# Kernel optimization log

Hardware: AMD Instinct MI355X
Metric: run time of the kernel (lower is better)

Reference implementation:

```python
import jax, jax.numpy as jnp
import numpy as np
import math

B, N, E, H, D = 8, 1024, 1024, 16, 64  # batch, node_cnt, embedding_dim, head_num, qkv_dim
SQRT_E, SQRT_D, CLIP = 32.0, 8.0, 10.0
MAX_PERIOD = 10000.0


def setup_inputs() -> dict:
    key = jax.random.key(0)
    ks = jax.random.split(key, 16)
    s = 0.03  # weight scale keeps tanh/softmax in a sane range
    return {
        "t": jax.random.uniform(ks[0], (B,), jnp.float32),
        "encoded_jobs": jax.random.normal(ks[1], (B, N, E), jnp.float32) * 0.5,
        "xt": jax.random.uniform(ks[2], (B, N, N), jnp.float32),
        "Wq": jax.random.normal(ks[3], (H * D, E), jnp.float32) * s,
        "Wk": jax.random.normal(ks[4], (H * D, E), jnp.float32) * s,
        "Wv": jax.random.normal(ks[5], (H * D, E), jnp.float32) * s,
        "Wc": jax.random.normal(ks[6], (E, H * D), jnp.float32) * s,
        "bc": jnp.zeros((E,), jnp.float32),
        "conv_w": jax.random.normal(ks[7], (2, 2), jnp.float32) * 0.5,  # 1x1 Conv2d(2,2)
        "conv_b": jnp.zeros((2,), jnp.float32),
        "tW1": jax.random.normal(ks[8], (E // 2, E), jnp.float32) * s,
        "tb1": jnp.zeros((E // 2,), jnp.float32),
        "tW2": jax.random.normal(ks[9], (E, E // 2), jnp.float32) * s,
        "tb2": jnp.zeros((E,), jnp.float32),
    }


def _timestep_embedding(t):
    half = E // 2
    freqs = jnp.exp(-math.log(MAX_PERIOD) * jnp.arange(half, dtype=jnp.float32) / half)
    args = t[:, None] * freqs[None, :]               # [B, E/2]
    return jnp.concatenate([jnp.cos(args), jnp.sin(args)], axis=-1)  # [B, E]


def reference(t, encoded_jobs, xt, Wq, Wk, Wv, Wc, bc, conv_w, conv_b, tW1, tb1, tW2, tb2):
    # time embedding MLP
    t_emb = jax.nn.relu(_timestep_embedding(t) @ tW1.T + tb1) @ tW2.T + tb2  # [B, E]

    def heads(W):
        return (encoded_jobs @ W.T).reshape(B, N, H, D).transpose(0, 2, 1, 3)  # [B,H,N,D]

    q, k, v = heads(Wq), heads(Wk), heads(Wv)
    attn = jax.nn.softmax(jnp.einsum('bhnd,bhmd->bhnm', q, k) / SQRT_D, axis=-1)
    out = jnp.einsum('bhnm,bhmd->bhnd', attn, v)
    out_concat = out.transpose(0, 2, 1, 3).reshape(B, N, H * D)
    mh = out_concat @ Wc.T + bc + t_emb[:, None, :]          # [B,N,E]

    # single-head score against encoded_jobs^T, scaled + tanh-clipped
    score = jnp.einsum('bne,bme->bnm', mh, encoded_jobs) / SQRT_E
    score_clipped = CLIP * jnp.tanh(score)

    stacked = jnp.stack([score_clipped, xt], axis=1)         # [B,2,N,N]
    conv_out = jnp.einsum('oi,binm->bonm', conv_w, stacked) + conv_b[None, :, None, None]
    return jax.nn.softmax(conv_out.transpose(0, 2, 3, 1), axis=3)  # [B,N,N,2]
```

## Files before the change

### kernel.cpp

```cpp
#include <hip/hip_runtime.h>
#include <hip/hip_bf16.h>
#include <math.h>

#define B_ 8
#define N_ 1024
#define E_ 1024
#define H_ 16
#define D_ 64

typedef __attribute__((ext_vector_type(8))) short short8;
typedef __attribute__((ext_vector_type(4))) float f32x4;

static __device__ __forceinline__ unsigned short f2bf(float f) {
    __hip_bfloat16 h = __float2bfloat16(f);
    return __builtin_bit_cast(unsigned short, h);
}
static __device__ __forceinline__ unsigned int cvtpk_bf16(float a, float b) {
    unsigned int r;
    asm("v_cvt_pk_bf16_f32 %0, %1, %2" : "=v"(r) : "v"(a), "v"(b));
    return r;
}
static __device__ __forceinline__ void gld_lds16(const void* g, void* l) {
    __builtin_amdgcn_global_load_lds(
        (const __attribute__((address_space(1))) unsigned int*)g,
        (__attribute__((address_space(3))) unsigned int*)l, 16, 0, 0);
}

__global__ __launch_bounds__(256) void cvt_fused(
    const float* __restrict__ ej, const float* __restrict__ w0,
    const float* __restrict__ w1, const float* __restrict__ w2,
    const float* __restrict__ w3,
    unsigned short* __restrict__ ejd, unsigned short* __restrict__ d0,
    unsigned short* __restrict__ d1, unsigned short* __restrict__ d2,
    unsigned short* __restrict__ d3,
    const float* __restrict__ t, const float* __restrict__ tW1,
    const float* __restrict__ tb1, float* __restrict__ h1T)
{
    const int gid = blockIdx.x;
    const int tid = threadIdx.x;
    if (gid < 12288) {
        const float* s; unsigned short* d; int i;
        if (gid < 8192) {
            s = ej; d = ejd; i = (gid * 256 + tid) * 4;
        } else {
            int w = (gid - 8192) >> 10;
            s = w == 0 ? w0 : (w == 1 ? w1 : (w == 2 ? w2 : w3));
            d = w == 0 ? d0 : (w == 1 ? d1 : (w == 2 ? d2 : d3));
            i = (((gid - 8192) & 1023) * 256 + tid) * 4;
        }
        float4 v = *(const float4*)(s + i);
        *(ushort4*)(d + i) = make_ushort4(f2bf(v.x), f2bf(v.y), f2bf(v.z), f2bf(v.w));
        return;
    }
    const int wv = tid >> 6, lane = tid & 63;
    const int j = (gid - 12288) * 4 + wv;
    float tv[8];
#pragma unroll
    for (int b = 0; b < 8; ++b) tv[b] = t[b];
    const float* w = tW1 + j * 1024;
    float acc[8];
#pragma unroll
    for (int b = 0; b < 8; ++b) acc[b] = 0.f;
    const float kLog = 9.210340371976184f;
    for (int e = lane; e < 1024; e += 64) {
        float we = w[e];
        int ef = e & 511;
        float freq = __expf(-kLog * (float)ef * (1.0f / 512.0f));
        if (e < 512) {
#pragma unroll
            for (int b = 0; b < 8; ++b) acc[b] = fmaf(we, __cosf(tv[b] * freq), acc[b]);
        } else {
#pragma unroll
            for (int b = 0; b < 8; ++b) acc[b] = fmaf(we, __sinf(tv[b] * freq), acc[b]);
        }
    }
#pragma unroll
    for (int off = 32; off > 0; off >>= 1)
#pragma unroll
        for (int b = 0; b < 8; ++b) acc[b] += __shfl_xor(acc[b], off, 64);
    if (lane == 0) {
        float bias = tb1[j];
#pragma unroll
        for (int b = 0; b < 8; ++b) h1T[j * 8 + b] = fmaxf(acc[b] + bias, 0.f);
    }
}

__global__ __launch_bounds__(256) void temb2_kernel(
    const float* __restrict__ h1T, const float* __restrict__ tW2,
    const float* __restrict__ tb2, float* __restrict__ temb)
{
    const int wv = threadIdx.x >> 6, lane = threadIdx.x & 63;
    const int e2 = blockIdx.x * 4 + wv;
    const float* w = tW2 + e2 * 512;
    float acc[8];
#pragma unroll
    for (int b = 0; b < 8; ++b) acc[b] = 0.f;
    for (int j = lane; j < 512; j += 64) {
        float wv_ = w[j];
        const float* hp = h1T + j * 8;
#pragma unroll
        for (int b = 0; b < 8; ++b) acc[b] = fmaf(hp[b], wv_, acc[b]);
    }
#pragma unroll
    for (int off = 32; off > 0; off >>= 1)
#pragma unroll
        for (int b = 0; b < 8; ++b) acc[b] += __shfl_xor(acc[b], off, 64);
    if (lane == 0) {
        float bias = tb2[e2];
#pragma unroll
        for (int b = 0; b < 8; ++b) temb[b * 1024 + e2] = acc[b] + bias;
    }
}

static __device__ __forceinline__ void gemm_loop(
    const unsigned short* __restrict__ A, const unsigned short* __restrict__ Bm,
    int m0, int n0, int K,
    unsigned short* As0, unsigned short* As1,
    unsigned short* Bs0, unsigned short* Bs1,
    f32x4 acc[4][4])
{
    const int tid = threadIdx.x;
    const int wave = tid >> 6, lane = tid & 63;
    const int wm = wave >> 1, wn = wave & 1;
    const int sr = lane >> 2, sc = (lane & 3) * 8;
    const unsigned short* Ag0 = A + (size_t)(m0 + wave * 16 + sr) * K + sc;
    const unsigned short* Ag1 = A + (size_t)(m0 + 64 + wave * 16 + sr) * K + sc;
    const unsigned short* Bg0 = Bm + (size_t)(n0 + wave * 16 + sr) * K + sc;
    const unsigned short* Bg1 = Bm + (size_t)(n0 + 64 + wave * 16 + sr) * K + sc;

    const f32x4 zero = {0.f, 0.f, 0.f, 0.f};
#pragma unroll
    for (int i = 0; i < 4; ++i)
#pragma unroll
        for (int j = 0; j < 4; ++j) acc[i][j] = zero;

    gld_lds16(Ag0, As0 + wave * 512);
    gld_lds16(Ag1, As0 + (wave + 4) * 512);
    gld_lds16(Bg0, Bs0 + wave * 512);
    gld_lds16(Bg1, Bs0 + (wave + 4) * 512);
    __syncthreads();

    const int fr = lane & 15, fq = (lane >> 4) * 8;
    int cur = 0;
    for (int k0 = 0; k0 < K; k0 += 32) {
        const unsigned short* sA = cur ? As1 : As0;
        const unsigned short* sB = cur ? Bs1 : Bs0;
        unsigned short* dA = cur ? As0 : As1;
        unsigned short* dB = cur ? Bs0 : Bs1;
        if (k0 + 32 < K) {
            gld_lds16(Ag0 + k0 + 32, dA + wave * 512);
            gld_lds16(Ag1 + k0 + 32, dA + (wave + 4) * 512);
            gld_lds16(Bg0 + k0 + 32, dB + wave * 512);
            gld_lds16(Bg1 + k0 + 32, dB + (wave + 4) * 512);
        }
        short8 af[4], bf[4];
#pragma unroll
        for (int i = 0; i < 4; ++i) {
            af[i] = *(const short8*)&sA[(wm * 64 + i * 16 + fr) * 32 + fq];
            bf[i] = *(const short8*)&sB[(wn * 64 + i * 16 + fr) * 32 + fq];
        }
#pragma unroll
        for (int i = 0; i < 4; ++i)
#pragma unroll
            for (int j = 0; j < 4; ++j)
                acc[i][j] = __builtin_amdgcn_mfma_f32_16x16x32_bf16(
                    af[i], bf[j], acc[i][j], 0, 0, 0);
        __syncthreads();
        cur ^= 1;
    }
}

static __device__ __forceinline__ void gemm_loop64(
    const unsigned short* __restrict__ A, const unsigned short* __restrict__ Bm,
    int m0, int n0, int K,
    unsigned short* As0, unsigned short* As1,
    unsigned short* Bs0, unsigned short* Bs1,
    f32x4 acc[2][4])
{
    const int tid = threadIdx.x;
    const int wave = tid >> 6, lane = tid & 63;
    const int wm = wave >> 1, wn = wave & 1;
    const int sr = lane >> 2, sc = (lane & 3) * 8;
    const unsigned short* Ag0 = A + (size_t)(m0 + wave * 16 + sr) * K + sc;
    const unsigned short* Bg0 = Bm + (size_t)(n0 + wave * 16 + sr) * K + sc;
    const unsigned short* Bg1 = Bm + (size_t)(n0 + 64 + wave * 16 + sr) * K + sc;

    const f32x4 zero = {0.f, 0.f, 0.f, 0.f};
#pragma unroll
    for (int i = 0; i < 2; ++i)
#pragma unroll
        for (int j = 0; j < 4; ++j) acc[i][j] = zero;

    gld_lds16(Ag0, As0 + wave * 512);
    gld_lds16(Bg0, Bs0 + wave * 512);
    gld_lds16(Bg1, Bs0 + (wave + 4) * 512);
    __syncthreads();

    const int fr = lane & 15, fq = (lane >> 4) * 8;
    int cur = 0;
    for (int k0 = 0; k0 < K; k0 += 32) {
        const unsigned short* sA = cur ? As1 : As0;
        const unsigned short* sB = cur ? Bs1 : Bs0;
        unsigned short* dA = cur ? As0 : As1;
        unsigned short* dB = cur ? Bs0 : Bs1;
        if (k0 + 32 < K) {
            gld_lds16(Ag0 + k0 + 32, dA + wave * 512);
            gld_lds16(Bg0 + k0 + 32, dB + wave * 512);
            gld_lds16(Bg1 + k0 + 32, dB + (wave + 4) * 512);
        }
        short8 af[2], bf[4];
#pragma unroll
        for (int i = 0; i < 2; ++i)
            af[i] = *(const short8*)&sA[(wm * 32 + i * 16 + fr) * 32 + fq];
#pragma unroll
        for (int j = 0; j < 4; ++j)
            bf[j] = *(const short8*)&sB[(wn * 64 + j * 16 + fr) * 32 + fq];
#pragma unroll
        for (int i = 0; i < 2; ++i)
#pragma unroll
            for (int j = 0; j < 4; ++j)
                acc[i][j] = __builtin_amdgcn_mfma_f32_16x16x32_bf16(
                    af[i], bf[j], acc[i][j], 0, 0, 0);
        __syncthreads();
        cur ^= 1;
    }
}

__global__ __launch_bounds__(256) void qkv_gemm(
    const unsigned short* __restrict__ A,
    const unsigned short* __restrict__ W0, const unsigned short* __restrict__ W1,
    const unsigned short* __restrict__ W2,
    unsigned short* __restrict__ C0, unsigned short* __restrict__ C1,
    unsigned short* __restrict__ C2)
{
    __shared__ unsigned short As0[128 * 32], As1[128 * 32];
    __shared__ unsigned short Bs0[128 * 32], Bs1[128 * 32];
    const int orig = blockIdx.x;
    const int sw = (orig & 7) * 192 + (orig >> 3);
    const int z = sw / 512, r = sw & 511;
    const int m0 = (r >> 3) * 128, n0 = (r & 7) * 128;
    const unsigned short* W = z == 0 ? W0 : (z == 1 ? W1 : W2);
    unsigned short* C = z == 0 ? C0 : (z == 1 ? C1 : C2);

    f32x4 acc[4][4];
    gemm_loop(A, W, m0, n0, 1024, As0, As1, Bs0, Bs1, acc);

    const int lane = threadIdx.x & 63, wave = threadIdx.x >> 6;
    const int wm = wave >> 1, wn = wave & 1;
    const int fr = lane & 15, fq4 = (lane >> 4) * 4;
#pragma unroll
    for (int i = 0; i < 4; ++i) {
        int row = m0 + wm * 64 + i * 16 + fq4;
#pragma unroll
        for (int j = 0; j < 4; ++j) {
            int col = n0 + wn * 64 + j * 16 + fr;
#pragma unroll
            for (int rr = 0; rr < 4; ++rr)
                C[(size_t)(row + rr) * 1024 + col] = f2bf(acc[i][j][rr]);
        }
    }
}

__global__ __launch_bounds__(256) void outproj_gemm(
    const unsigned short* __restrict__ A, const unsigned short* __restrict__ Bm,
    unsigned short* __restrict__ C,
    const float* __restrict__ bias, const float* __restrict__ temb)
{
    __shared__ unsigned short As0[64 * 32], As1[64 * 32];
    __shared__ unsigned short Bs0[128 * 32], Bs1[128 * 32];
    const int orig = blockIdx.x;
    const int sw = (orig & 7) * 128 + (orig >> 3);
    const int mt = sw >> 3, n0 = (sw & 7) * 128;
    const int m0 = mt * 64;

    f32x4 acc[2][4];
    gemm_loop64(A, Bm, m0, n0, 1024, As0, As1, Bs0, Bs1, acc);

    const int lane = threadIdx.x & 63, wave = threadIdx.x >> 6;
    const int wm = wave >> 1, wn = wave & 1;
    const int fr = lane & 15, fq4 = (lane >> 4) * 4;
    const int bb = m0 >> 10;
#pragma unroll
    for (int i = 0; i < 2; ++i) {
        int row = m0 + wm * 32 + i * 16 + fq4;
#pragma unroll
        for (int j = 0; j < 4; ++j) {
            int col = n0 + wn * 64 + j * 16 + fr;
            float epi = bias[col] + temb[bb * 1024 + col];
#pragma unroll
            for (int rr = 0; rr < 4; ++rr)
                C[(size_t)(row + rr) * 1024 + col] = f2bf(acc[i][j][rr] + epi);
        }
    }
}

__global__ __launch_bounds__(256, 2) void attn_mfma(
    const unsigned short* __restrict__ Q, const unsigned short* __restrict__ K,
    const unsigned short* __restrict__ V, unsigned short* __restrict__ O)
{
    __shared__ __align__(16) unsigned short Ks[64 * 72];
    __shared__ __align__(16) unsigned short Vts[80 * 72];
    const int tid = threadIdx.x;
    const int wq = tid >> 6, lane = tid & 63;
    const int lo = lane & 15, hi = lane >> 4;
    const int id = blockIdx.x;
    const int sw = (id & 7) * 64 + (id >> 3);
    const int q0 = (sw & 3) * 256;
    const int h = (sw >> 2) & 15, b = sw >> 6;
    const size_t base = ((size_t)b * N_) * 1024 + h * 64;

    for (int i = tid; i < 16 * 64; i += 256) {
        int rr = i >> 6, cc = i & 63;
        Vts[(64 + rr) * 72 + cc] = (rr == 0) ? (unsigned short)0x3F80 : (unsigned short)0;
    }
    __syncthreads();
    short8 vb4[2];
#pragma unroll
    for (int k2 = 0; k2 < 2; ++k2)
        vb4[k2] = *(const short8*)&Vts[(64 + lo) * 72 + hi * 8 + k2 * 32];

    short8 aq[4][2];
#pragma unroll
    for (int qt = 0; qt < 4; ++qt)
#pragma unroll
        for (int ks = 0; ks < 2; ++ks)
            aq[qt][ks] = *(const short8*)(Q + base +
                (size_t)(q0 + wq * 64 + qt * 16 + lo) * 1024 + hi * 8 + ks * 32);

    f32x4 o_[4][5];
    const f32x4 zero = {0.f, 0.f, 0.f, 0.f};
#pragma unroll
    for (int qt = 0; qt < 4; ++qt)
#pragma unroll
        for (int db = 0; db < 5; ++db) o_[qt][db] = zero;

    const int kr = tid >> 2, ku = (tid & 3) * 16;
    const unsigned short* Kg = K + base + (size_t)kr * 1024 + ku;
    const int vkv = (tid & 31) * 2, vd = (tid >> 5) * 8;
    const int scol = (vkv & 0x23) | ((vkv & 0x0C) << 1) | ((vkv & 0x10) >> 2);
    const unsigned short* Vg = V + base + (size_t)vkv * 1024 + vd;

    short8 kl0 = *(const short8*)(Kg);
    short8 kl1 = *(const short8*)(Kg + 8);
    short8 vla = *(const short8*)(Vg);
    short8 vlb = *(const short8*)(Vg + 1024);

    const float cexp = 0.1803368801111204f;

    for (int kt = 0; kt < N_; kt += 64) {
        __syncthreads();
        *(short8*)&Ks[kr * 72 + ku] = kl0;
        *(short8*)&Ks[kr * 72 + ku + 8] = kl1;
#pragma unroll
        for (int i = 0; i < 8; ++i) {
            unsigned int pv = (unsigned int)(unsigned short)vla[i] |
                              ((unsigned int)(unsigned short)vlb[i] << 16);
            *(unsigned int*)&Vts[(vd + i) * 72 + scol] = pv;
        }
        __syncthreads();
        if (kt + 64 < N_) {
            kl0 = *(const short8*)(Kg + (size_t)(kt + 64) * 1024);
            kl1 = *(const short8*)(Kg + (size_t)(kt + 64) * 1024 + 8);
            vla = *(const short8*)(Vg + (size_t)(kt + 64) * 1024);
            vlb = *(const short8*)(Vg + (size_t)(kt + 64) * 1024 + 1024);
        }

        short8 kb[4][2], vb[4][2];
#pragma unroll
        for (int jk = 0; jk < 4; ++jk)
#pragma unroll
            for (int ks = 0; ks < 2; ++ks)
                kb[jk][ks] = *(const short8*)&Ks[(16 * jk + lo) * 72 + hi * 8 + ks * 32];
#pragma unroll
        for (int db = 0; db < 4; ++db)
#pragma unroll
            for (int k2 = 0; k2 < 2; ++k2)
                vb[db][k2] = *(const short8*)&Vts[(16 * db + lo) * 72 +
                                                  hi * 8 + k2 * 32];

#pragma unroll
        for (int qt = 0; qt < 4; ++qt) {
            f32x4 s[4];
            __builtin_amdgcn_s_setprio(1);
#pragma unroll
            for (int jk = 0; jk < 4; ++jk) {
                s[jk] = __builtin_amdgcn_mfma_f32_16x16x32_bf16(
                    kb[jk][0], aq[qt][0], zero, 0, 0, 0);
                s[jk] = __builtin_amdgcn_mfma_f32_16x16x32_bf16(
                    kb[jk][1], aq[qt][1], s[jk], 0, 0, 0);
            }
            __builtin_amdgcn_s_setprio(0);
#pragma unroll
            for (int jk = 0; jk < 4; ++jk)
#pragma unroll
                for (int rr = 0; rr < 4; ++rr)
                    s[jk][rr] = exp2f(s[jk][rr] * cexp);
            unsigned int pw[8];
#pragma unroll
            for (int jk = 0; jk < 4; ++jk) {
                pw[2 * jk] = cvtpk_bf16(s[jk][0], s[jk][1]);
                pw[2 * jk + 1] = cvtpk_bf16(s[jk][2], s[jk][3]);
            }
            uint4 pa0 = make_uint4(pw[0], pw[1], pw[2], pw[3]);
            uint4 pa1 = make_uint4(pw[4], pw[5], pw[6], pw[7]);
            short8 pA = __builtin_bit_cast(short8, pa0);
            short8 pB = __builtin_bit_cast(short8, pa1);

            __builtin_amdgcn_s_setprio(1);
#pragma unroll
            for (int db = 0; db < 4; ++db) {
                o_[qt][db] = __builtin_amdgcn_mfma_f32_16x16x32_bf16(
                    vb[db][0], pA, o_[qt][db], 0, 0, 0);
                o_[qt][db] = __builtin_amdgcn_mfma_f32_16x16x32_bf16(
                    vb[db][1], pB, o_[qt][db], 0, 0, 0);
            }
            o_[qt][4] = __builtin_amdgcn_mfma_f32_16x16x32_bf16(
                vb4[0], pA, o_[qt][4], 0, 0, 0);
            o_[qt][4] = __builtin_amdgcn_mfma_f32_16x16x32_bf16(
                vb4[1], pB, o_[qt][4], 0, 0, 0);
            __builtin_amdgcn_s_setprio(0);
        }
    }

#pragma unroll
    for (int qt = 0; qt < 4; ++qt) {
        float lsum = __shfl(o_[qt][4][0], lo, 64);
        float inv = 1.f / lsum;
        const size_t rb = base + (size_t)(q0 + wq * 64 + qt * 16 + lo) * 1024;
#pragma unroll
        for (int db = 0; db < 4; ++db) {
            *(ushort4*)(O + rb + 16 * db + 4 * hi) = make_ushort4(
                f2bf(o_[qt][db][0] * inv), f2bf(o_[qt][db][1] * inv),
                f2bf(o_[qt][db][2] * inv), f2bf(o_[qt][db][3] * inv));
        }
    }
}

__global__ __launch_bounds__(256) void score_bf16(
    const unsigned short* __restrict__ MH, const unsigned short* __restrict__ EJ,
    const float* __restrict__ xt, const float* __restrict__ convw,
    const float* __restrict__ convb, float* __restrict__ out)
{
    __shared__ unsigned short As0[64 * 32], As1[64 * 32];
    __shared__ unsigned short Bs0[128 * 32], Bs1[128 * 32];
    const int orig = blockIdx.x;
    const int sw = (orig & 7) * 128 + (orig >> 3);
    const int bz = sw >> 7;
    const int m0 = ((sw >> 3) & 15) * 64, n0 = (sw & 7) * 128;
    const unsigned short* A = MH + (size_t)bz * N_ * E_;
    const unsigned short* Bm = EJ + (size_t)bz * N_ * E_;

    f32x4 acc[2][4];
    gemm_loop64(A, Bm, m0, n0, 1024, As0, As1, Bs0, Bs1, acc);

    const int lane = threadIdx.x & 63, wave = threadIdx.x >> 6;
    const int wm = wave >> 1, wn = wave & 1;
    const int fr = lane & 15, fq4 = (lane >> 4) * 4;
    const float w00 = convw[0], w01 = convw[1], w10 = convw[2], w11 = convw[3];
    const float cb0 = convb[0], cb1 = convb[1];
    const float L2E = 1.4426950408889634f;
    const float kT = -2.f * L2E * 0.03125f;
#pragma unroll
    for (int i = 0; i < 2; ++i) {
#pragma unroll
        for (int rr = 0; rr < 4; ++rr) {
            int row = m0 + wm * 32 + i * 16 + fq4 + rr;
            const float* xrow = xt + ((size_t)bz * N_ + row) * N_;
            float2* orow = (float2*)(out + (((size_t)bz * N_ + row) * N_) * 2);
#pragma unroll
            for (int j = 0; j < 4; ++j) {
                int col = n0 + wn * 64 + j * 16 + fr;
                float e = exp2f(acc[i][j][rr] * kT);
                float sc_ = fmaf(20.f, 1.f / (1.f + e), -10.f);
                float x = xrow[col];
                float c0 = fmaf(w00, sc_, fmaf(w01, x, cb0));
                float c1 = fmaf(w10, sc_, fmaf(w11, x, cb1));
                float e1 = exp2f((c1 - c0) * L2E);
                float o0 = 1.f / (1.f + e1);
                orow[col] = make_float2(o0, 1.f - o0);
            }
        }
    }
}

extern "C" void kernel_launch(void* const* d_in, const int* in_sizes, int n_in,
                              void* d_out, int out_size, void* d_ws, size_t ws_size,
                              hipStream_t stream)
{
    (void)in_sizes; (void)n_in; (void)out_size; (void)ws_size;
    const float* t     = (const float*)d_in[0];
    const float* ej    = (const float*)d_in[1];
    const float* xt    = (const float*)d_in[2];
    const float* Wq    = (const float*)d_in[3];
    const float* Wk    = (const float*)d_in[4];
    const float* Wv    = (const float*)d_in[5];
    const float* Wc    = (const float*)d_in[6];
    const float* bc    = (const float*)d_in[7];
    const float* convw = (const float*)d_in[8];
    const float* convb = (const float*)d_in[9];
    const float* tW1   = (const float*)d_in[10];
    const float* tb1   = (const float*)d_in[11];
    const float* tW2   = (const float*)d_in[12];
    const float* tb2   = (const float*)d_in[13];
    float* out = (float*)d_out;

    const size_t SZ = (size_t)B_ * N_ * 1024;
    float* ws = (float*)d_ws;
    float* temb = ws;
    float* h1T  = ws + 8192;
    unsigned short* ej_bf = (unsigned short*)(ws + 8192 + 4096);
    unsigned short* MH_bf = ej_bf + SZ;
    unsigned short* Wq_bf = MH_bf + SZ;
    unsigned short* Wk_bf = Wq_bf + (size_t)E_ * 1024;
    unsigned short* Wv_bf = Wk_bf + (size_t)E_ * 1024;
    unsigned short* Wc_bf = Wv_bf + (size_t)E_ * 1024;

    unsigned short* Qb = (unsigned short*)d_out;
    unsigned short* Kb = Qb + SZ;
    unsigned short* Vb = Kb + SZ;
    unsigned short* Ob = Vb + SZ;

    cvt_fused<<<dim3(12416), dim3(256), 0, stream>>>(
        ej, Wq, Wk, Wv, Wc, ej_bf, Wq_bf, Wk_bf, Wv_bf, Wc_bf,
        t, tW1, tb1, h1T);
    temb2_kernel<<<dim3(256), dim3(256), 0, stream>>>(h1T, tW2, tb2, temb);

    dim3 gblk(256);
    qkv_gemm<<<dim3(1536), gblk, 0, stream>>>(
        ej_bf, Wq_bf, Wk_bf, Wv_bf, Qb, Kb, Vb);

    attn_mfma<<<dim3(512), gblk, 0, stream>>>(Qb, Kb, Vb, Ob);

    outproj_gemm<<<dim3(1024), gblk, 0, stream>>>(Ob, Wc_bf, MH_bf, bc, temb);

    score_bf16<<<dim3(1024), gblk, 0, stream>>>(
        MH_bf, ej_bf, xt, convw, convb, out);
}
```

Baseline: 207.6 us.

## Double-buffer K/V tiles in attention and use fast reciprocal in epilogues

The attention kernel now keeps two LDS buffers for K and V. The next tile is written while the current one is computed, which removes one barrier per 64-key step. The ones-row used for the softmax denominator moves to its own small LDS array. Raw v_rcp_f32 replaces IEEE division in the attention normalisation and in the score tanh/softmax epilogue, trading a little precision for cheaper instructions. The extra LDS could reduce occupancy, though launch bounds already cap it at 2 blocks per CU.

```diff
diff --git a/kernel.cpp b/kernel.cpp
--- a/kernel.cpp
+++ b/kernel.cpp
@@ -18,6 +18,11 @@
 static __device__ __forceinline__ unsigned int cvtpk_bf16(float a, float b) {
     unsigned int r;
     asm("v_cvt_pk_bf16_f32 %0, %1, %2" : "=v"(r) : "v"(a), "v"(b));
+    return r;
+}
+static __device__ __forceinline__ float fast_rcp(float x) {
+    float r;
+    asm("v_rcp_f32 %0, %1" : "=v"(r) : "v"(x));
     return r;
 }
 static __device__ __forceinline__ void gld_lds16(const void* g, void* l) {
@@ -298,8 +303,9 @@
     const unsigned short* __restrict__ Q, const unsigned short* __restrict__ K,
     const unsigned short* __restrict__ V, unsigned short* __restrict__ O)
 {
-    __shared__ __align__(16) unsigned short Ks[64 * 72];
-    __shared__ __align__(16) unsigned short Vts[80 * 72];
+    __shared__ __align__(16) unsigned short Ks[2][64 * 72];
+    __shared__ __align__(16) unsigned short Vts[2][64 * 72];
+    __shared__ __align__(16) unsigned short Vone[16 * 72];
     const int tid = threadIdx.x;
     const int wq = tid >> 6, lane = tid & 63;
     const int lo = lane & 15, hi = lane >> 4;
@@ -311,13 +317,8 @@
 
     for (int i = tid; i < 16 * 64; i += 256) {
         int rr = i >> 6, cc = i & 63;
-        Vts[(64 + rr) * 72 + cc] = (rr == 0) ? (unsigned short)0x3F80 : (unsigned short)0;
-    }
-    __syncthreads();
-    short8 vb4[2];
-#pragma unroll
-    for (int k2 = 0; k2 < 2; ++k2)
-        vb4[k2] = *(const short8*)&Vts[(64 + lo) * 72 + hi * 8 + k2 * 32];
+        Vone[rr * 72 + cc] = (rr == 0) ? (unsigned short)0x3F80 : (unsigned short)0;
+    }
 
     short8 aq[4][2];
 #pragma unroll
@@ -340,43 +341,33 @@
     const int scol = (vkv & 0x23) | ((vkv & 0x0C) << 1) | ((vkv & 0x10) >> 2);
     const unsigned short* Vg = V + base + (size_t)vkv * 1024 + vd;
 
-    short8 kl0 = *(const short8*)(Kg);
-    short8 kl1 = *(const short8*)(Kg + 8);
-    short8 vla = *(const short8*)(Vg);
-    short8 vlb = *(const short8*)(Vg + 1024);
-
     const float cexp = 0.1803368801111204f;
 
-    for (int kt = 0; kt < N_; kt += 64) {
-        __syncthreads();
-        *(short8*)&Ks[kr * 72 + ku] = kl0;
-        *(short8*)&Ks[kr * 72 + ku + 8] = kl1;
+    auto write_tile = [&](unsigned short* KB, unsigned short* VB,
+                          short8 k0, short8 k1, short8 va, short8 vb_) {
+        *(short8*)&KB[kr * 72 + ku] = k0;
+        *(short8*)&KB[kr * 72 + ku + 8] = k1;
 #pragma unroll
         for (int i = 0; i < 8; ++i) {
-            unsigned int pv = (unsigned int)(unsigned short)vla[i] |
-                              ((unsigned int)(unsigned short)vlb[i] << 16);
-            *(unsigned int*)&Vts[(vd + i) * 72 + scol] = pv;
-        }
-        __syncthreads();
-        if (kt + 64 < N_) {
-            kl0 = *(const short8*)(Kg + (size_t)(kt + 64) * 1024);
-            kl1 = *(const short8*)(Kg + (size_t)(kt + 64) * 1024 + 8);
-            vla = *(const short8*)(Vg + (size_t)(kt + 64) * 1024);
-            vlb = *(const short8*)(Vg + (size_t)(kt + 64) * 1024 + 1024);
-        }
-
+            unsigned int pv = (unsigned int)(unsigned short)va[i] |
+                              ((unsigned int)(unsigned short)vb_[i] << 16);
+            *(unsigned int*)&VB[(vd + i) * 72 + scol] = pv;
+        }
+    };
+
+    short8 vb4[2];
+    auto compute_tile = [&](const unsigned short* KB, const unsigned short* VB) {
         short8 kb[4][2], vb[4][2];
 #pragma unroll
         for (int jk = 0; jk < 4; ++jk)
 #pragma unroll
             for (int ks = 0; ks < 2; ++ks)
-                kb[jk][ks] = *(const short8*)&Ks[(16 * jk + lo) * 72 + hi * 8 + ks * 32];
+                kb[jk][ks] = *(const short8*)&KB[(16 * jk + lo) * 72 + hi * 8 + ks * 32];
 #pragma unroll
         for (int db = 0; db < 4; ++db)
 #pragma unroll
             for (int k2 = 0; k2 < 2; ++k2)
-                vb[db][k2] = *(const short8*)&Vts[(16 * db + lo) * 72 +
-                                                  hi * 8 + k2 * 32];
+                vb[db][k2] = *(const short8*)&VB[(16 * db + lo) * 72 + hi * 8 + k2 * 32];
 
 #pragma unroll
         for (int qt = 0; qt < 4; ++qt) {
@@ -420,12 +411,50 @@
                 vb4[1], pB, o_[qt][4], 0, 0, 0);
             __builtin_amdgcn_s_setprio(0);
         }
+    };
+
+    short8 kA0 = *(const short8*)(Kg);
+    short8 kA1 = *(const short8*)(Kg + 8);
+    short8 vAa = *(const short8*)(Vg);
+    short8 vAb = *(const short8*)(Vg + 1024);
+    write_tile(Ks[0], Vts[0], kA0, kA1, vAa, vAb);
+    short8 kB0 = *(const short8*)(Kg + (size_t)64 * 1024);
+    short8 kB1 = *(const short8*)(Kg + (size_t)64 * 1024 + 8);
+    short8 vBa = *(const short8*)(Vg + (size_t)64 * 1024);
+    short8 vBb = *(const short8*)(Vg + (size_t)64 * 1024 + 1024);
+    __syncthreads();
+#pragma unroll
+    for (int k2 = 0; k2 < 2; ++k2)
+        vb4[k2] = *(const short8*)&Vone[lo * 72 + hi * 8 + k2 * 32];
+
+    for (int kt = 0; kt < N_; kt += 128) {
+        if (kt + 128 < N_) {
+            kA0 = *(const short8*)(Kg + (size_t)(kt + 128) * 1024);
+            kA1 = *(const short8*)(Kg + (size_t)(kt + 128) * 1024 + 8);
+            vAa = *(const short8*)(Vg + (size_t)(kt + 128) * 1024);
+            vAb = *(const short8*)(Vg + (size_t)(kt + 128) * 1024 + 1024);
+        }
+        write_tile(Ks[1], Vts[1], kB0, kB1, vBa, vBb);
+        compute_tile(Ks[0], Vts[0]);
+        __syncthreads();
+
+        if (kt + 192 < N_) {
+            kB0 = *(const short8*)(Kg + (size_t)(kt + 192) * 1024);
+            kB1 = *(const short8*)(Kg + (size_t)(kt + 192) * 1024 + 8);
+            vBa = *(const short8*)(Vg + (size_t)(kt + 192) * 1024);
+            vBb = *(const short8*)(Vg + (size_t)(kt + 192) * 1024 + 1024);
+        }
+        if (kt + 128 < N_)
+            write_tile(Ks[0], Vts[0], kA0, kA1, vAa, vAb);
+        compute_tile(Ks[1], Vts[1]);
+        if (kt + 128 < N_)
+            __syncthreads();
     }
 
 #pragma unroll
     for (int qt = 0; qt < 4; ++qt) {
         float lsum = __shfl(o_[qt][4][0], lo, 64);
-        float inv = 1.f / lsum;
+        float inv = fast_rcp(lsum);
         const size_t rb = base + (size_t)(q0 + wq * 64 + qt * 16 + lo) * 1024;
 #pragma unroll
         for (int db = 0; db < 4; ++db) {
@@ -471,12 +500,12 @@
             for (int j = 0; j < 4; ++j) {
                 int col = n0 + wn * 64 + j * 16 + fr;
                 float e = exp2f(acc[i][j][rr] * kT);
-                float sc_ = fmaf(20.f, 1.f / (1.f + e), -10.f);
+                float sc_ = fmaf(20.f, fast_rcp(1.f + e), -10.f);
                 float x = xrow[col];
                 float c0 = fmaf(w00, sc_, fmaf(w01, x, cb0));
                 float c1 = fmaf(w10, sc_, fmaf(w11, x, cb1));
                 float e1 = exp2f((c1 - c0) * L2E);
-                float o0 = 1.f / (1.f + e1);
+                float o0 = fast_rcp(1.f + e1);
                 orow[col] = make_float2(o0, 1.f - o0);
             }
         }
```

New measurement: 209.6 us. About the same (+1.0%).
